# Performance work log

Hardware: AMD Instinct MI355X
Metric: run time of the kernel (lower is better)

Reference implementation:

```python
import jax, jax.numpy as jnp
import numpy as np

DIM = 768
HEADS = 12
HEAD_DIM = DIM // HEADS  # 64
SCALE = HEAD_DIM ** -0.5
B, H, W = 16, 64, 64
EPS_BN = 1e-5
EPS_SQRT = 1e-5


def setup_inputs() -> dict:
    key = jax.random.key(0)
    k0, k1, k2, k3, k4 = jax.random.split(key, 5)
    x = jax.random.normal(k0, (B, DIM, H, W), dtype=jnp.float32)
    # 1x1 conv == pointwise matmul over channels
    qkv_w = jax.random.normal(k1, (3 * DIM, DIM), dtype=jnp.float32) * (DIM ** -0.5)
    qkv_b = jax.random.normal(k2, (3 * DIM,), dtype=jnp.float32) * 0.01
    gamma = 1.0 + 0.1 * jax.random.normal(k3, (DIM,), dtype=jnp.float32)
    beta = 0.1 * jax.random.normal(k4, (DIM,), dtype=jnp.float32)
    return {"x": x, "qkv_w": qkv_w, "qkv_b": qkv_b, "gamma": gamma, "beta": beta}


def reference(x, qkv_w, qkv_b, gamma, beta):
    b, c, h, w = x.shape
    n = h * w
    xf = x.reshape(b, c, n)  # [B, C, N]
    # qkv 1x1 conv
    qkv = jnp.einsum('oc,bcn->bon', qkv_w, xf) + qkv_b[None, :, None]  # [B, 3C, N]
    qkv = qkv.reshape(b, 3, HEADS, HEAD_DIM, n)
    q, k, v = qkv[:, 0], qkv[:, 1], qkv[:, 2]  # each [B, h, d, N]
    # channel attention: contract over N -> [B, h, d, d]
    attn = jnp.einsum('bhdn,bhen->bhde', q, k) * SCALE
    attn = jnp.sign(attn) * jnp.sqrt(jnp.abs(attn) + EPS_SQRT)
    attn = jax.nn.softmax(attn, axis=-1)
    # BatchNorm2d (training-mode batch statistics, biased variance) + ReLU
    mean = jnp.mean(x, axis=(0, 2, 3))
    var = jnp.var(x, axis=(0, 2, 3))
    y = (x - mean[None, :, None, None]) * jax.lax.rsqrt(var + EPS_BN)[None, :, None, None]
    y = y * gamma[None, :, None, None] + beta[None, :, None, None]
    out = jnp.maximum(y, 0.0)
    # original module discards attn; returned here so the attention math is
    return out, attn
```

## Files before the change

### kernel.cpp

```cpp
#include <hip/hip_runtime.h>
#include <hip/hip_bf16.h>

#define DIM 768
#define NB 16
#define NPOS 4096
#define HEADS 12

typedef unsigned short u16;
typedef __attribute__((ext_vector_type(4))) float f32x4;
typedef __attribute__((ext_vector_type(8))) short s16x8;
typedef __attribute__((ext_vector_type(4))) u16 u16x4;

static __device__ __forceinline__ u16 f2bf(float f) {
  __hip_bfloat16 h = __float2bfloat16(f);
  u16 u; __builtin_memcpy(&u, &h, 2); return u;
}
static __device__ __forceinline__ float bf2f(u16 u) {
  unsigned int x = ((unsigned int)u) << 16;
  float f; __builtin_memcpy(&f, &x, 4); return f;
}

static __device__ __forceinline__ int lds_idx(int row, int slotf) {
  return row * 64 + (((slotf) ^ (row & 7)) << 3);
}


__global__ __launch_bounds__(128) void sums_cast_kernel(const float* __restrict__ x,
                                                        float* __restrict__ sum_bc,
                                                        float* __restrict__ sumsq_bc,
                                                        u16* __restrict__ Xb) {
  int bc = blockIdx.x;
  const float4* p = (const float4*)(x + (size_t)bc * NPOS);
  u16x4* ob = (u16x4*)(Xb + (size_t)bc * NPOS);
  int t = threadIdx.x;
  float s = 0.f, ss = 0.f;
  for (int i = t; i < NPOS / 4; i += 128) {
    float4 v = p[i];
    s  += v.x + v.y + v.z + v.w;
    ss += v.x * v.x + v.y * v.y + v.z * v.z + v.w * v.w;
    u16x4 hv = {f2bf(v.x), f2bf(v.y), f2bf(v.z), f2bf(v.w)};
    ob[i] = hv;
  }
  for (int off = 32; off; off >>= 1) { s += __shfl_down(s, off); ss += __shfl_down(ss, off); }
  __shared__ float red[4];
  int lane = t & 63, w = t >> 6;
  if (lane == 0) { red[w] = s; red[2 + w] = ss; }
  __syncthreads();
  if (t == 0) { sum_bc[bc] = red[0] + red[1]; sumsq_bc[bc] = red[2] + red[3]; }
}

__global__ void finalize_kernel(const float* __restrict__ sum_bc, const float* __restrict__ sumsq_bc,
                                const float* __restrict__ gamma, const float* __restrict__ beta,
                                float* __restrict__ chanScale, float* __restrict__ chanShift) {
  int c = blockIdx.x * blockDim.x + threadIdx.x;
  if (c >= DIM) return;
  float s = 0.f, ss = 0.f;
  for (int b = 0; b < NB; b++) { s += sum_bc[b * DIM + c]; ss += sumsq_bc[b * DIM + c]; }
  const float invn = 1.f / ((float)NB * (float)NPOS);
  float mean = s * invn;
  float var  = ss * invn - mean * mean;
  float rstd = rsqrtf(var + 1e-5f);
  float a = rstd * gamma[c];
  chanScale[c] = a;
  chanShift[c] = beta[c] - mean * a;
}

__global__ __launch_bounds__(256) void bn_kernel(const float* __restrict__ x,
                                                 const float* __restrict__ chanScale,
                                                 const float* __restrict__ chanShift,
                                                 float* __restrict__ out) {
  const size_t n4 = (size_t)NB * DIM * NPOS / 4;
  const float4* x4 = (const float4*)x;
  float4* o4 = (float4*)out;
  for (size_t i = (size_t)blockIdx.x * blockDim.x + threadIdx.x; i < n4;
       i += (size_t)gridDim.x * blockDim.x) {
    float4 v = x4[i];
    int c = (int)((i >> 10) % DIM);
    float a = chanScale[c], sh = chanShift[c];
    v.x = fmaxf(fmaf(v.x, a, sh), 0.f);
    v.y = fmaxf(fmaf(v.y, a, sh), 0.f);
    v.z = fmaxf(fmaf(v.z, a, sh), 0.f);
    v.w = fmaxf(fmaf(v.w, a, sh), 0.f);
    o4[i] = v;
  }
}


__global__ __launch_bounds__(64) void tvecw_kernel(const float* __restrict__ W,
                                                   const float* __restrict__ sum_bc,
                                                   float* __restrict__ tvec,
                                                   u16* __restrict__ Wb) {
  int r = blockIdx.x;
  int lane = threadIdx.x;
  const float* wr = W + (size_t)r * DIM;
  float acc[NB];
#pragma unroll
  for (int b = 0; b < NB; b++) acc[b] = 0.f;
#pragma unroll
  for (int j = 0; j < DIM / 64; j++) {
    int c = lane + j * 64;
    float wv = wr[c];
    Wb[(size_t)r * DIM + c] = f2bf(wv);
#pragma unroll
    for (int b = 0; b < NB; b++) acc[b] += wv * sum_bc[b * DIM + c];
  }
#pragma unroll
  for (int b = 0; b < NB; b++) {
    float v = acc[b];
    for (int off = 32; off; off >>= 1) v += __shfl_down(v, off);
    if (lane == 0) tvec[(size_t)b * 1536 + r] = v;
  }
}


template <bool SYMM>
__global__ __launch_bounds__(256) void gemm_kernel(
    const u16* __restrict__ A, long long strideA,
    const u16* __restrict__ B, long long strideB,
    u16* __restrict__ C, long long strideC,
    int lda, int ldb, int ldc, int K, int nGram,
    const u16* __restrict__ XbBn, const float* __restrict__ chanScale,
    const float* __restrict__ chanShift, float* __restrict__ outY) {
  __shared__ __align__(16) u16 As[2][128 * 64];
  __shared__ __align__(16) u16 Bs[2][128 * 64];

  int ti, tj, bz;
  if (SYMM) {
    if ((int)blockIdx.x >= nGram) {
      int t = threadIdx.x;
      const size_t total8 = (size_t)NB * DIM * NPOS / 8;
      size_t stride = (size_t)(gridDim.x - nGram) * 256;
      const s16x8* xs = (const s16x8*)XbBn;
      float4* o4 = (float4*)outY;
      for (size_t i = (size_t)(blockIdx.x - nGram) * 256 + t; i < total8; i += stride) {
        s16x8 v = xs[i];
        int c = (int)((i >> 9) % DIM);
        float a = chanScale[c], sh = chanShift[c];
        float4 o0, o1;
        o0.x = fmaxf(fmaf(bf2f((u16)v[0]), a, sh), 0.f);
        o0.y = fmaxf(fmaf(bf2f((u16)v[1]), a, sh), 0.f);
        o0.z = fmaxf(fmaf(bf2f((u16)v[2]), a, sh), 0.f);
        o0.w = fmaxf(fmaf(bf2f((u16)v[3]), a, sh), 0.f);
        o1.x = fmaxf(fmaf(bf2f((u16)v[4]), a, sh), 0.f);
        o1.y = fmaxf(fmaf(bf2f((u16)v[5]), a, sh), 0.f);
        o1.z = fmaxf(fmaf(bf2f((u16)v[6]), a, sh), 0.f);
        o1.w = fmaxf(fmaf(bf2f((u16)v[7]), a, sh), 0.f);
        o4[2 * i] = o0;
        o4[2 * i + 1] = o1;
      }
      return;
    }
    int bid = blockIdx.x;
    int swz = (bid & 7) * 42 + (bid >> 3);
    bz = swz / 21;
    int idx = swz % 21, rem = 6;
    ti = 0;
    while (idx >= rem) { idx -= rem; ti++; rem--; }
    tj = ti + idx;
  } else {
    ti = blockIdx.x; tj = blockIdx.y; bz = blockIdx.z;
  }
  const u16* Ab = A + (size_t)bz * strideA;
  const u16* Bb = B + (size_t)bz * strideB;
  u16* Cb = C + (size_t)bz * strideC;
  int ib = ti * 128, jb = tj * 128;

  int t = threadIdx.x, lane = t & 63;
  int w = t >> 6;
  int wr = (w >> 1) * 64, wc = (w & 1) * 64;
  int fr = lane & 15, q4 = lane >> 4;
  int srow = t >> 3;
  int sslot = t & 7;
  int wslot = sslot ^ (srow & 7);

  const u16* Asrc = Ab + (size_t)(ib + srow) * lda + sslot * 8;
  const u16* Bsrc = Bb + (size_t)(jb + srow) * ldb + sslot * 8;
  int lw = srow * 64 + wslot * 8;

  f32x4 acc[4][4];
#pragma unroll
  for (int m = 0; m < 4; m++)
#pragma unroll
    for (int n = 0; n < 4; n++) acc[m][n] = (f32x4){0.f, 0.f, 0.f, 0.f};

  s16x8 rA[4], rB[4];

#define GLOAD(k0)                                                               \
  {                                                                             \
    _Pragma("unroll")                                                           \
    for (int p = 0; p < 4; p++) {                                               \
      rA[p] = *(const s16x8*)(Asrc + (size_t)(p * 32) * lda + (k0));            \
      rB[p] = *(const s16x8*)(Bsrc + (size_t)(p * 32) * ldb + (k0));            \
    }                                                                           \
  }

#define DSW(buf)                                                                \
  {                                                                             \
    _Pragma("unroll")                                                           \
    for (int p = 0; p < 4; p++) {                                               \
      *(s16x8*)&As[buf][lw + p * 2048] = rA[p];                                 \
      *(s16x8*)&Bs[buf][lw + p * 2048] = rB[p];                                 \
    }                                                                           \
  }

#define COMPUTE(buf)                                                            \
  {                                                                             \
    _Pragma("unroll")                                                           \
    for (int kk = 0; kk < 2; kk++) {                                            \
      int sbase = kk * 4 + q4;                                                  \
      s16x8 af[4], bfv[4];                                                      \
      _Pragma("unroll")                                                         \
      for (int m = 0; m < 4; m++) af[m] = *(const s16x8*)&As[buf][lds_idx(wr + m * 16 + fr, sbase)]; \
      _Pragma("unroll")                                                         \
      for (int n = 0; n < 4; n++) bfv[n] = *(const s16x8*)&Bs[buf][lds_idx(wc + n * 16 + fr, sbase)]; \
      _Pragma("unroll")                                                         \
      for (int m = 0; m < 4; m++)                                               \
        _Pragma("unroll")                                                       \
        for (int n = 0; n < 4; n++)                                             \
          acc[m][n] = __builtin_amdgcn_mfma_f32_16x16x32_bf16(af[m], bfv[n], acc[m][n], 0, 0, 0); \
    }                                                                           \
  }

  const int nt = K >> 6;
  GLOAD(0);
  DSW(0);
  GLOAD(64);
  asm volatile("s_waitcnt lgkmcnt(0)" ::: "memory");
  __builtin_amdgcn_s_barrier();
  __builtin_amdgcn_sched_barrier(0);
  for (int t2 = 0; t2 < nt; t2 += 2) {
    COMPUTE(0);
    DSW(1);
    if (t2 + 2 < nt) GLOAD((t2 + 2) << 6);
    asm volatile("s_waitcnt lgkmcnt(0)" ::: "memory");
    __builtin_amdgcn_s_barrier();
    __builtin_amdgcn_sched_barrier(0);
    COMPUTE(1);
    if (t2 + 2 < nt) {
      DSW(0);
      if (t2 + 3 < nt) GLOAD((t2 + 3) << 6);
    }
    asm volatile("s_waitcnt lgkmcnt(0)" ::: "memory");
    __builtin_amdgcn_s_barrier();
    __builtin_amdgcn_sched_barrier(0);
  }
#undef GLOAD
#undef DSW
#undef COMPUTE

  int rbase = q4 * 4;
#pragma unroll
  for (int m = 0; m < 4; m++)
#pragma unroll
    for (int n = 0; n < 4; n++)
#pragma unroll
      for (int r = 0; r < 4; r++) {
        int row = ib + wr + m * 16 + rbase + r;
        int col = jb + wc + n * 16 + fr;
        u16 v = f2bf(acc[m][n][r]);
        Cb[(size_t)row * ldc + col] = v;
        if (SYMM && ti != tj) Cb[(size_t)col * ldc + row] = v;
      }
}


__global__ __launch_bounds__(256) void attn_kernel(const u16* __restrict__ Pb,
                                                   const u16* __restrict__ Wb,
                                                   const float* __restrict__ bias,
                                                   const float* __restrict__ tvec,
                                                   float* __restrict__ outAttn) {
  int h = blockIdx.x, b = blockIdx.y;
  __shared__ __align__(16) u16 As[2][64 * 64];
  __shared__ __align__(16) u16 Bs[2][64 * 64];
  __shared__ float sm[64 * 65];
  const u16* Pa = Pb + ((size_t)b * DIM + h * 64) * DIM;
  const u16* Wk = Wb + (size_t)(DIM + h * 64) * DIM;

  int t = threadIdx.x, lane = t & 63, w = t >> 6;
  int fr = lane & 15, q4 = lane >> 4;
  int srow = t >> 3;
  int sslot = t & 7;
  int wslot = sslot ^ (srow & 7);

  const u16* Asrc = Pa + (size_t)srow * DIM + sslot * 8;
  const u16* Bsrc = Wk + (size_t)srow * DIM + sslot * 8;
  int lw = srow * 64 + wslot * 8;

  f32x4 acc[4];
#pragma unroll
  for (int n = 0; n < 4; n++) acc[n] = (f32x4){0.f, 0.f, 0.f, 0.f};

  s16x8 rA[2], rB[2];

#define AGLOAD(k0)                                                              \
  {                                                                             \
    _Pragma("unroll")                                                           \
    for (int p = 0; p < 2; p++) {                                               \
      rA[p] = *(const s16x8*)(Asrc + (size_t)(p * 32) * DIM + (k0));            \
      rB[p] = *(const s16x8*)(Bsrc + (size_t)(p * 32) * DIM + (k0));            \
    }                                                                           \
  }

#define ADSW(buf)                                                               \
  {                                                                             \
    _Pragma("unroll")                                                           \
    for (int p = 0; p < 2; p++) {                                               \
      *(s16x8*)&As[buf][lw + p * 2048] = rA[p];                                 \
      *(s16x8*)&Bs[buf][lw + p * 2048] = rB[p];                                 \
    }                                                                           \
  }

#define ACOMPUTE(buf)                                                           \
  {                                                                             \
    _Pragma("unroll")                                                           \
    for (int kk = 0; kk < 2; kk++) {                                            \
      int sbase = kk * 4 + q4;                                                  \
      s16x8 af = *(const s16x8*)&As[buf][lds_idx(w * 16 + fr, sbase)];          \
      _Pragma("unroll")                                                         \
      for (int n = 0; n < 4; n++) {                                             \
        s16x8 bfv = *(const s16x8*)&Bs[buf][lds_idx(n * 16 + fr, sbase)];       \
        acc[n] = __builtin_amdgcn_mfma_f32_16x16x32_bf16(af, bfv, acc[n], 0, 0, 0); \
      }                                                                         \
    }                                                                           \
  }

  AGLOAD(0);
  ADSW(0);
  AGLOAD(64);
  asm volatile("s_waitcnt lgkmcnt(0)" ::: "memory");
  __builtin_amdgcn_s_barrier();
  __builtin_amdgcn_sched_barrier(0);
  for (int t2 = 0; t2 < 12; t2 += 2) {
    ACOMPUTE(0);
    ADSW(1);
    if (t2 + 2 < 12) AGLOAD((t2 + 2) << 6);
    asm volatile("s_waitcnt lgkmcnt(0)" ::: "memory");
    __builtin_amdgcn_s_barrier();
    __builtin_amdgcn_sched_barrier(0);
    ACOMPUTE(1);
    if (t2 + 2 < 12) {
      ADSW(0);
      if (t2 + 3 < 12) AGLOAD((t2 + 3) << 6);
    }
    asm volatile("s_waitcnt lgkmcnt(0)" ::: "memory");
    __builtin_amdgcn_s_barrier();
    __builtin_amdgcn_sched_barrier(0);
  }
#undef AGLOAD
#undef ADSW
#undef ACOMPUTE

  const float* tq = tvec + (size_t)b * 1536 + h * 64;
  const float* tk = tq + DIM;
  const float* bq = bias + h * 64;
  const float* bk = bias + DIM + h * 64;
  int rbase = q4 * 4;
#pragma unroll
  for (int n = 0; n < 4; n++) {
    int e = n * 16 + fr;
    float bke = bk[e], tke = tk[e];
#pragma unroll
    for (int r = 0; r < 4; r++) {
      int d = w * 16 + rbase + r;
      float bqd = bq[d];
      float raw = acc[n][r] + bqd * tke + bke * tq[d] + 4096.f * bqd * bke;
      float val = 0.125f * raw;
      float sq = sqrtf(fabsf(val) + 1e-5f);
      sm[d * 65 + e] = val > 0.f ? sq : (val < 0.f ? -sq : 0.f);
    }
  }
  __syncthreads();
  {
    int d = t >> 2, qd = (t & 3) * 16;
    const float* row = &sm[d * 65];
    float mx = -1e30f;
#pragma unroll
    for (int e2 = 0; e2 < 16; e2++) mx = fmaxf(mx, row[qd + e2]);
    mx = fmaxf(mx, __shfl_xor(mx, 1));
    mx = fmaxf(mx, __shfl_xor(mx, 2));
    float sum = 0.f;
#pragma unroll
    for (int e2 = 0; e2 < 16; e2++) sum += __expf(row[qd + e2] - mx);
    sum += __shfl_xor(sum, 1);
    sum += __shfl_xor(sum, 2);
    float inv = 1.f / sum;
    float* o = outAttn + (((size_t)b * HEADS + h) * 64 + d) * 64;
#pragma unroll
    for (int e2 = 0; e2 < 16; e2++) o[qd + e2] = __expf(row[qd + e2] - mx) * inv;
  }
}


extern "C" void kernel_launch(void* const* d_in, const int* in_sizes, int n_in,
                              void* d_out, int out_size, void* d_ws, size_t ws_size,
                              hipStream_t stream) {
  const float* x     = (const float*)d_in[0];
  const float* qkv_w = (const float*)d_in[1];
  const float* qkv_b = (const float*)d_in[2];
  const float* gamma = (const float*)d_in[3];
  const float* beta  = (const float*)d_in[4];
  float* out = (float*)d_out;
  float* ws  = (float*)d_ws;

  float* sum_bc    = ws;
  float* sumsq_bc  = ws + 12288;
  float* chanScale = ws + 24576;
  float* chanShift = ws + 25344;
  float* tvec      = ws + 26112;
  u16* Wb = (u16*)(ws + 50688);
  u16* Gb = (u16*)((char*)d_ws + 2562048);
  u16* Pb = (u16*)((char*)d_ws + 2562048 + 18874368);

  const bool wsRoom = ws_size >= (41943040ull + 100663296ull + 1024ull);
  u16* Xb = wsRoom ? (u16*)((char*)d_ws + 41943040) : (u16*)d_out;

  sums_cast_kernel<<<NB * DIM, 128, 0, stream>>>(x, sum_bc, sumsq_bc, Xb);
  finalize_kernel<<<3, 256, 0, stream>>>(sum_bc, sumsq_bc, gamma, beta, chanScale, chanShift);
  tvecw_kernel<<<2 * DIM, 64, 0, stream>>>(qkv_w, sum_bc, tvec, Wb);

  if (wsRoom) {
    gemm_kernel<true><<<336 + 256, 256, 0, stream>>>(
        Xb, (long long)DIM * NPOS, Xb, (long long)DIM * NPOS, Gb, (long long)DIM * DIM,
        NPOS, NPOS, DIM, NPOS, 336, Xb, chanScale, chanShift, out);
  } else {
    gemm_kernel<true><<<336, 256, 0, stream>>>(
        Xb, (long long)DIM * NPOS, Xb, (long long)DIM * NPOS, Gb, (long long)DIM * DIM,
        NPOS, NPOS, DIM, NPOS, 336, nullptr, chanScale, chanShift, nullptr);
    bn_kernel<<<2048, 256, 0, stream>>>(x, chanScale, chanShift, out);
  }

  gemm_kernel<false><<<dim3(6, 6, NB), 256, 0, stream>>>(
      Wb, 0LL, Gb, (long long)DIM * DIM, Pb, (long long)DIM * DIM,
      DIM, DIM, DIM, DIM, 1 << 30, nullptr, nullptr, nullptr, nullptr);

  attn_kernel<<<dim3(HEADS, NB), 256, 0, stream>>>(Pb, Wb, qkv_b, tvec,
                                                   out + (size_t)NB * DIM * NPOS);
}
```

Measured before the change: 254.9 us.

## Fuse Gram GEMM and BN output into one cooperative kernel with phased grid syncs

Replaces the combined Gram-matrix GEMM plus BatchNorm/ReLU launch with a cooperative kernel of 512 blocks. 336 blocks do symmetric Gram tiles and 176 blocks stream the BN output, with XCD-aware block mapping. Both roles advance in four phases separated by grid.sync, so the memory-bound BN writes are interleaved with MFMA work instead of competing unevenly. The cost is four grid-wide barriers, where the slowest role stalls the other. It relies on all 512 blocks being co-resident and falls back to the old path if the cooperative launch fails.

```diff
diff --git a/kernel.cpp b/kernel.cpp
--- a/kernel.cpp
+++ b/kernel.cpp
@@ -1,5 +1,8 @@
 #include <hip/hip_runtime.h>
 #include <hip/hip_bf16.h>
+#include <hip/hip_cooperative_groups.h>
+
+namespace cg = cooperative_groups;
 
 #define DIM 768
 #define NB 16
@@ -110,6 +113,159 @@
     for (int off = 32; off; off >>= 1) v += __shfl_down(v, off);
     if (lane == 0) tvec[(size_t)b * 1536 + r] = v;
   }
+}
+
+
+__global__ __launch_bounds__(256) void gram_bn_coop(
+    const u16* __restrict__ X, u16* __restrict__ G,
+    const float* __restrict__ chanScale, const float* __restrict__ chanShift,
+    float* __restrict__ outY) {
+  cg::grid_group grid = cg::this_grid();
+  __shared__ __align__(16) u16 As[2][128 * 64];
+  __shared__ __align__(16) u16 Bs[2][128 * 64];
+
+  int bid = blockIdx.x;
+  int xcd = bid & 7, ix = bid >> 3;
+
+  if (ix >= 42) {
+    int bnid = xcd * 22 + (ix - 42);
+    int t = threadIdx.x;
+    const size_t per = (size_t)NB * DIM * NPOS / 8 / 4;
+    const s16x8* xs = (const s16x8*)X;
+    f32x4* o4 = (f32x4*)outY;
+    const size_t stride = (size_t)176 * 256;
+    for (int c = 0; c < 4; c++) {
+      if (c) grid.sync();
+      size_t lo = per * c, hi = lo + per;
+      for (size_t i = lo + (size_t)bnid * 256 + t; i < hi; i += stride) {
+        s16x8 v = __builtin_nontemporal_load(xs + i);
+        int ch = (int)((i >> 9) % DIM);
+        float a = chanScale[ch], sh = chanShift[ch];
+        f32x4 o0, o1;
+        o0[0] = fmaxf(fmaf(bf2f((u16)v[0]), a, sh), 0.f);
+        o0[1] = fmaxf(fmaf(bf2f((u16)v[1]), a, sh), 0.f);
+        o0[2] = fmaxf(fmaf(bf2f((u16)v[2]), a, sh), 0.f);
+        o0[3] = fmaxf(fmaf(bf2f((u16)v[3]), a, sh), 0.f);
+        o1[0] = fmaxf(fmaf(bf2f((u16)v[4]), a, sh), 0.f);
+        o1[1] = fmaxf(fmaf(bf2f((u16)v[5]), a, sh), 0.f);
+        o1[2] = fmaxf(fmaf(bf2f((u16)v[6]), a, sh), 0.f);
+        o1[3] = fmaxf(fmaf(bf2f((u16)v[7]), a, sh), 0.f);
+        __builtin_nontemporal_store(o0, o4 + 2 * i);
+        __builtin_nontemporal_store(o1, o4 + 2 * i + 1);
+      }
+    }
+    return;
+  }
+
+  int g = xcd * 42 + ix;
+  int bz = g / 21;
+  int idx = g % 21, rem = 6, ti = 0;
+  while (idx >= rem) { idx -= rem; ti++; rem--; }
+  int tj = ti + idx;
+
+  const u16* Xb = X + (size_t)bz * DIM * NPOS;
+  u16* Cb = G + (size_t)bz * DIM * DIM;
+  int ib = ti * 128, jb = tj * 128;
+
+  int t = threadIdx.x, lane = t & 63;
+  int w = t >> 6;
+  int wr = (w >> 1) * 64, wc = (w & 1) * 64;
+  int fr = lane & 15, q4 = lane >> 4;
+  int srow = t >> 3;
+  int sslot = t & 7;
+  int wslot = sslot ^ (srow & 7);
+
+  const u16* Asrc = Xb + (size_t)(ib + srow) * NPOS + sslot * 8;
+  const u16* Bsrc = Xb + (size_t)(jb + srow) * NPOS + sslot * 8;
+  int lw = srow * 64 + wslot * 8;
+
+  f32x4 acc[4][4];
+#pragma unroll
+  for (int m = 0; m < 4; m++)
+#pragma unroll
+    for (int n = 0; n < 4; n++) acc[m][n] = (f32x4){0.f, 0.f, 0.f, 0.f};
+
+  s16x8 rA[4], rB[4];
+
+#define GLOAD(k0)                                                               \
+  {                                                                             \
+    _Pragma("unroll")                                                           \
+    for (int p = 0; p < 4; p++) {                                               \
+      rA[p] = *(const s16x8*)(Asrc + (size_t)(p * 32) * NPOS + (k0));           \
+      rB[p] = *(const s16x8*)(Bsrc + (size_t)(p * 32) * NPOS + (k0));           \
+    }                                                                           \
+  }
+
+#define DSW(buf)                                                                \
+  {                                                                             \
+    _Pragma("unroll")                                                           \
+    for (int p = 0; p < 4; p++) {                                               \
+      *(s16x8*)&As[buf][lw + p * 2048] = rA[p];                                 \
+      *(s16x8*)&Bs[buf][lw + p * 2048] = rB[p];                                 \
+    }                                                                           \
+  }
+
+#define COMPUTE(buf)                                                            \
+  {                                                                             \
+    _Pragma("unroll")                                                           \
+    for (int kk = 0; kk < 2; kk++) {                                            \
+      int sbase = kk * 4 + q4;                                                  \
+      s16x8 af[4], bfv[4];                                                      \
+      _Pragma("unroll")                                                         \
+      for (int m = 0; m < 4; m++) af[m] = *(const s16x8*)&As[buf][lds_idx(wr + m * 16 + fr, sbase)]; \
+      _Pragma("unroll")                                                         \
+      for (int n = 0; n < 4; n++) bfv[n] = *(const s16x8*)&Bs[buf][lds_idx(wc + n * 16 + fr, sbase)]; \
+      _Pragma("unroll")                                                         \
+      for (int m = 0; m < 4; m++)                                               \
+        _Pragma("unroll")                                                       \
+        for (int n = 0; n < 4; n++)                                             \
+          acc[m][n] = __builtin_amdgcn_mfma_f32_16x16x32_bf16(af[m], bfv[n], acc[m][n], 0, 0, 0); \
+    }                                                                           \
+  }
+
+  const int nt = 64;
+  GLOAD(0);
+  DSW(0);
+  GLOAD(64);
+  asm volatile("s_waitcnt lgkmcnt(0)" ::: "memory");
+  __builtin_amdgcn_s_barrier();
+  __builtin_amdgcn_sched_barrier(0);
+  for (int c = 0; c < 4; c++) {
+    if (c) grid.sync();
+    for (int t2 = c * 16; t2 < c * 16 + 16; t2 += 2) {
+      COMPUTE(0);
+      DSW(1);
+      if (t2 + 2 < nt) GLOAD((t2 + 2) << 6);
+      asm volatile("s_waitcnt lgkmcnt(0)" ::: "memory");
+      __builtin_amdgcn_s_barrier();
+      __builtin_amdgcn_sched_barrier(0);
+      COMPUTE(1);
+      if (t2 + 2 < nt) {
+        DSW(0);
+        if (t2 + 3 < nt) GLOAD((t2 + 3) << 6);
+      }
+      asm volatile("s_waitcnt lgkmcnt(0)" ::: "memory");
+      __builtin_amdgcn_s_barrier();
+      __builtin_amdgcn_sched_barrier(0);
+    }
+  }
+#undef GLOAD
+#undef DSW
+#undef COMPUTE
+
+  int rbase = q4 * 4;
+#pragma unroll
+  for (int m = 0; m < 4; m++)
+#pragma unroll
+    for (int n = 0; n < 4; n++)
+#pragma unroll
+      for (int r = 0; r < 4; r++) {
+        int row = ib + wr + m * 16 + rbase + r;
+        int col = jb + wc + n * 16 + fr;
+        u16 v = f2bf(acc[m][n][r]);
+        Cb[(size_t)row * DIM + col] = v;
+        if (ti != tj) Cb[(size_t)col * DIM + row] = v;
+      }
 }
 
 
@@ -418,15 +574,25 @@
   finalize_kernel<<<3, 256, 0, stream>>>(sum_bc, sumsq_bc, gamma, beta, chanScale, chanShift);
   tvecw_kernel<<<2 * DIM, 64, 0, stream>>>(qkv_w, sum_bc, tvec, Wb);
 
+  bool coopDone = false;
   if (wsRoom) {
-    gemm_kernel<true><<<336 + 256, 256, 0, stream>>>(
-        Xb, (long long)DIM * NPOS, Xb, (long long)DIM * NPOS, Gb, (long long)DIM * DIM,
-        NPOS, NPOS, DIM, NPOS, 336, Xb, chanScale, chanShift, out);
-  } else {
-    gemm_kernel<true><<<336, 256, 0, stream>>>(
-        Xb, (long long)DIM * NPOS, Xb, (long long)DIM * NPOS, Gb, (long long)DIM * DIM,
-        NPOS, NPOS, DIM, NPOS, 336, nullptr, chanScale, chanShift, nullptr);
-    bn_kernel<<<2048, 256, 0, stream>>>(x, chanScale, chanShift, out);
+    void* args[] = {(void*)&Xb, (void*)&Gb, (void*)&chanScale, (void*)&chanShift,
+                    (void*)&out};
+    hipError_t e = hipLaunchCooperativeKernel((const void*)gram_bn_coop,
+                                              dim3(512), dim3(256), args, 0, stream);
+    coopDone = (e == hipSuccess);
+  }
+  if (!coopDone) {
+    if (wsRoom) {
+      gemm_kernel<true><<<336 + 256, 256, 0, stream>>>(
+          Xb, (long long)DIM * NPOS, Xb, (long long)DIM * NPOS, Gb, (long long)DIM * DIM,
+          NPOS, NPOS, DIM, NPOS, 336, Xb, chanScale, chanShift, out);
+    } else {
+      gemm_kernel<true><<<336, 256, 0, stream>>>(
+          Xb, (long long)DIM * NPOS, Xb, (long long)DIM * NPOS, Gb, (long long)DIM * DIM,
+          NPOS, NPOS, DIM, NPOS, 336, nullptr, chanScale, chanShift, nullptr);
+      bn_kernel<<<2048, 256, 0, stream>>>(x, chanScale, chanShift, out);
+    }
   }
 
   gemm_kernel<false><<<dim3(6, 6, NB), 256, 0, stream>>>(
```

Result: slower. 481.9 us (+89.1%).
